# Optimization experiments

Measured on AMD Instinct MI355X. Metric: run time of the kernel, lower is better.

The kernel has to match this reference:

```python
import jax, jax.numpy as jnp
import numpy as np

N = 524288      # number of outer 'batch' steps (acts as the time axis)
S = 1           # inner seq_len
SPIN = 1000
TRAIN = 400000
ML = 2.9086     # hard-coded PET normalizer mean
SL = 1.898      # hard-coded PET normalizer std
SCALE_MR = 500.0


def setup_inputs() -> dict:
    key = jax.random.key(0)
    ks = jax.random.split(key, 16)
    u = lambda k, shape: jax.random.uniform(k, shape, dtype=jnp.float32)
    return {
        "x": u(ks[0], (N, S, 2)),
        "y_obs": u(ks[1], (N, 1)),
        "p_mean": u(ks[2], (1,)),
        "p_std": u(ks[3], (1,)) + 0.5,  # keep away from zero (divisor)
        "weight_r_yom": u(ks[4], (1, 1)),
        "weight_r_ylm": u(ks[5], (1, 1)),
        "weight_r_yfm": u(ks[6], (1, 1)),
        "weight_r_yvm": u(ks[7], (1, 1)),
        "bias_b0_yom": u(ks[8], (1,)),
        "weight_b1_yom": u(ks[9], (1, 1)),
        "bias_b0_ylm": u(ks[10], (1,)),
        "weight_b2_ylm": u(ks[11], (1, 1)),
        "bias_b0_yrm": u(ks[12], (1,)),
        "epoch": 1,       # unused by the forward math
        "time_lag": 0,
    }


def _forward(x, y_obs, p_mean, p_std,
             weight_r_yom, weight_r_ylm, weight_r_yfm, weight_r_yvm,
             bias_b0_yom, weight_b1_yom, bias_b0_ylm, weight_b2_ylm,
             bias_b0_yrm, time_lag):
    n, s, _ = x.shape
    mo = p_mean[0]
    so = p_std[0]
    # hidden_size == 1: all [1,1] matmuls are scalar multiplies
    wb1 = weight_b1_yom[0, 0]
    wb2 = weight_b2_ylm[0, 0]
    b0_yom = bias_b0_yom[0]
    b0_ylm = bias_b0_ylm[0]
    thr = jnp.exp(bias_b0_yrm[0])
    eo = jnp.exp(weight_r_yom[0, 0])
    el = jnp.exp(weight_r_ylm[0, 0])
    ef = jnp.exp(weight_r_yfm[0, 0])
    den = eo + el + ef
    oo1 = eo / den
    ol1 = el / den
    svm = jax.nn.sigmoid(weight_r_yvm[0, 0])

    def cell(c0, u):
        u1, u2 = u[0], u[1]
        oo = oo1 * jax.nn.sigmoid(b0_yom + (c0 - mo) / so * wb1)
        ol = ol1 * jax.nn.sigmoid(b0_ylm + (u2 - ML) / SL * wb2)
        pos = c0 > 0
        safe_c0 = jnp.where(pos, c0, 1.0)
        olc = jnp.where(pos, ol - jax.nn.relu(ol - u2 / safe_c0), ol)
        f = 1.0 - oo - olc
        ov1 = svm * jnp.sign(c0 / SCALE_MR - thr)
        ov = ov1 - jax.nn.relu(ov1 - f)
        c1 = f * c0 + u1 - ov * jnp.abs(c0 - thr * SCALE_MR)
        # recorded quantities use the PRE-update state c0 (as in the torch code)
        outs = jnp.stack([oo * c0, c0, ol * c0, olc * c0, oo, ol, olc, f, ov])
        return c1, outs

    def body(c0, inp_b):
        xb, active = inp_b          # xb: [S,2]
        c1, outs_seq = jax.lax.scan(cell, c0, xb)
        outs = jnp.where(active, outs_seq[-1], 0.0)
        c_next = jnp.where(active, c1, c0)
        return c_next, outs

    active = jnp.arange(n) >= time_lag
    _, O = jax.lax.scan(body, jnp.float32(0.0), (x, active))  # O: [N,9]

    h_n = O[:, 0:1]
    c_n = O[:, 1:2]
    l_n = O[:, 2:3]
    lc_n = O[:, 3:4]
    Gate_oo = O[:, 4:5]
    Gate_ol = O[:, 5:6]
    Gate_olc = O[:, 6:7]
    Gate_f = O[:, 7:8]
    Gate_ov = O[:, 8:9]
    zeros = jnp.zeros_like(h_n)   # bp_n and Gate_ib (ib == 0)
    obsstd = jnp.std(y_obs[SPIN:TRAIN], ddof=1)  # torch.std is unbiased
    obs_std = jnp.where(active[:, None], obsstd, 0.0).astype(x.dtype)
    h_nout = jnp.concatenate([h_n, obs_std], axis=1)
    return (h_n, c_n, l_n, lc_n, zeros, zeros, Gate_oo, Gate_ol, Gate_olc,
            Gate_f, h_nout, obs_std, Gate_ov)


def reference(x, y_obs, p_mean, p_std,
              weight_r_yom, weight_r_ylm, weight_r_yfm, weight_r_yvm,
              bias_b0_yom, weight_b1_yom, bias_b0_ylm, weight_b2_ylm,
              bias_b0_yrm, epoch, time_lag):
    del epoch  # unused by the module's math
    return _forward(x, y_obs, p_mean, p_std,
                    weight_r_yom, weight_r_ylm, weight_r_yfm, weight_r_yvm,
                    bias_b0_yom, weight_b1_yom, bias_b0_ylm, weight_b2_ylm,
                    bias_b0_yrm, time_lag)
```

## Files before the change

### kernel.cpp

```cpp
#include <hip/hip_runtime.h>
#include <math.h>

#define SPIN_  1000
#define TRAIN_ 400000
#define ML_    2.9086f
#define SL_    1.898f
#define SCALE_MR_ 500.0f

#define CHUNK 8
#define BURN  96
#define BLOCK_T 64
#define TILE  (BLOCK_T * CHUNK)
#define WLEN  (TILE + BURN)
#define WPAD  (WLEN + WLEN / 16 + 1)
#define RED_BLOCKS 128
#define AGG_BLOCK  RED_BLOCKS

#define MAGIC_TICKET 0xF00DF00DF00DF00DULL
#define MAGIC_HI     0x5AF00D5AU

__device__ __forceinline__ float rcp_(float x) { return __builtin_amdgcn_rcpf(x); }
__device__ __forceinline__ float sigf_(float x) { return rcp_(1.0f + __expf(-x)); }

struct Params {
    float oo1, ol1, svm, thr, T, k1, a1, k2, a2;
};

__device__ __forceinline__ void step_(float c, float u1, float u2, const Params& P,
                                      float& oo, float& ol, float& olc, float& f,
                                      float& ov, float& c1) {
    oo = P.oo1 * sigf_(fmaf(c, P.k1, P.a1));
    ol = P.ol1 * sigf_(fmaf(u2, P.k2, P.a2));
    float q = u2 * rcp_(c);
    olc = (c > 0.0f) ? fminf(ol, q) : ol;
    f = 1.0f - oo - olc;
    float s = fmaf(c, 1.0f / SCALE_MR_, -P.thr);
    float sg = (s > 0.0f) ? 1.0f : ((s < 0.0f) ? -1.0f : 0.0f);
    ov = fminf(P.svm * sg, f);
    c1 = f * c + u1 - ov * (SCALE_MR_ * fabsf(s));
}

#define ROWP (CHUNK + 1)
#define SSTR (BLOCK_T * ROWP)

__global__ __launch_bounds__(BLOCK_T)
void mcpbrnn_fused_kernel(const float2* __restrict__ x,
                          const float* __restrict__ y,
                          float* __restrict__ out,
                          unsigned long long* __restrict__ W,
                          const float* __restrict__ p_mean,
                          const float* __restrict__ p_std,
                          const float* __restrict__ w_r_yom,
                          const float* __restrict__ w_r_ylm,
                          const float* __restrict__ w_r_yfm,
                          const float* __restrict__ w_r_yvm,
                          const float* __restrict__ b0_yom_p,
                          const float* __restrict__ w_b1_yom,
                          const float* __restrict__ b0_ylm_p,
                          const float* __restrict__ w_b2_ylm,
                          const float* __restrict__ b0_yrm_p,
                          const int* __restrict__ time_lag_p,
                          int n) {
    __shared__ float xu1[WPAD];
    __shared__ float xu2[WPAD];
    __shared__ float lds[9 * SSTR];

    const int tid = threadIdx.x;
    const int bid = blockIdx.x;
    const int base = bid * TILE;
    const int n0 = base + tid * CHUNK;
    const int tl = time_lag_p[0];
    const int N = n;

    if (bid < RED_BLOCKS) {
        const float4* y4 = (const float4*)(y + SPIN_);
        const int n4 = (TRAIN_ - SPIN_) / 4;
        const int per = (n4 + RED_BLOCKS - 1) / RED_BLOCKS;
        int s0 = bid * per;
        int e0 = s0 + per; if (e0 > n4) e0 = n4;
        double s = 0.0, q = 0.0;
        for (int i = s0 + tid; i < e0; i += BLOCK_T) {
            float4 v = y4[i];
            double a = (double)v.x, b = (double)v.y, c = (double)v.z, d = (double)v.w;
            s += a + b + c + d;
            q += a * a + b * b + c * c + d * d;
        }
#pragma unroll
        for (int o = 32; o > 0; o >>= 1) {
            s += __shfl_down(s, o, 64);
            q += __shfl_down(q, o, 64);
        }
        if (tid == 0) {
            atomicExch(&W[2 * bid],     (unsigned long long)__double_as_longlong(s));
            atomicExch(&W[2 * bid + 1], (unsigned long long)__double_as_longlong(q));
            __threadfence();
            atomicExch(&W[256 + bid], MAGIC_TICKET);
        }
    }

    {
        const int f4base = (base - BURN) >> 1;
        for (int k = tid; k < WLEN / 2; k += BLOCK_T) {
            int gk = f4base + k;
            float4 v;
            if (gk >= 0 && 2 * gk + 1 < N) {
                v = ((const float4*)x)[gk];
            } else {
                int i0 = 2 * gk;     if (i0 < 0) i0 = 0; if (i0 > N - 1) i0 = N - 1;
                int i1 = 2 * gk + 1; if (i1 < 0) i1 = 0; if (i1 > N - 1) i1 = N - 1;
                float2 a = x[i0];
                float2 b = x[i1];
                v = make_float4(a.x, a.y, b.x, b.y);
            }
            int p = 2 * k;
            int pp = p + (p >> 4);
            xu1[pp] = v.x; xu2[pp] = v.y;
            int p1 = p + 1;
            int pp1 = p1 + (p1 >> 4);
            xu1[pp1] = v.z; xu2[pp1] = v.w;
        }
    }

    Params P;
    {
        float mo = p_mean[0];
        float so = p_std[0];
        float wb1 = w_b1_yom[0];
        float wb2 = w_b2_ylm[0];
        float b0_yom = b0_yom_p[0];
        float b0_ylm = b0_ylm_p[0];
        P.thr = __expf(b0_yrm_p[0]);
        float eo = __expf(w_r_yom[0]);
        float el = __expf(w_r_ylm[0]);
        float ef = __expf(w_r_yfm[0]);
        float den = eo + el + ef;
        P.oo1 = eo / den;
        P.ol1 = el / den;
        P.svm = sigf_(w_r_yvm[0]);
        P.T = P.thr * SCALE_MR_;
        P.k1 = wb1 / so;
        P.a1 = b0_yom - mo * P.k1;
        P.k2 = wb2 / SL_;
        P.a2 = b0_ylm - ML_ * P.k2;
    }

    __syncthreads();

    const bool full_tile = (base + TILE <= N);
    const bool thread_active = (n0 < N);
    const int pbase = tid * CHUNK;
    const int row = tid * ROWP;

    const int gb0 = n0 - BURN;
    int jthr = tl - gb0; if (jthr < 0) jthr = 0;

    if (thread_active) {
        float c = 0.0f;
#pragma unroll 8
        for (int j = 0; j < BURN; ++j) {
            int p = pbase + j;
            int pp = p + (p >> 4);
            float u1 = xu1[pp];
            float u2 = xu2[pp];
            float oo, ol, olc, f, ov, c1;
            step_(c, u1, u2, P, oo, ol, olc, f, ov, c1);
            c = (j >= jthr) ? c1 : c;
        }

#pragma unroll
        for (int j = 0; j < CHUNK; ++j) {
            int gi = n0 + j;
            if (gi < N) {
                int p = pbase + BURN + j;
                int pp = p + (p >> 4);
                float u1 = xu1[pp];
                float u2 = xu2[pp];
                float oo, ol, olc, f, ov, c1;
                step_(c, u1, u2, P, oo, ol, olc, f, ov, c1);
                bool act = (BURN + j) >= jthr;
                float h = oo * c;
                if (full_tile) {
                    int idx = row + j;
                    lds[0 * SSTR + idx] = act ? h        : 0.0f;
                    lds[1 * SSTR + idx] = act ? c        : 0.0f;
                    lds[2 * SSTR + idx] = act ? ol * c   : 0.0f;
                    lds[3 * SSTR + idx] = act ? olc * c  : 0.0f;
                    lds[4 * SSTR + idx] = act ? oo       : 0.0f;
                    lds[5 * SSTR + idx] = act ? ol       : 0.0f;
                    lds[6 * SSTR + idx] = act ? olc      : 0.0f;
                    lds[7 * SSTR + idx] = act ? f        : 0.0f;
                    lds[8 * SSTR + idx] = act ? ov       : 0.0f;
                } else {
                    float hv = act ? h : 0.0f;
                    out[gi]            = hv;
                    out[N + gi]        = act ? c : 0.0f;
                    out[2 * N + gi]    = act ? ol * c : 0.0f;
                    out[3 * N + gi]    = act ? olc * c : 0.0f;
                    out[4 * N + gi]    = 0.0f;
                    out[5 * N + gi]    = 0.0f;
                    out[6 * N + gi]    = act ? oo : 0.0f;
                    out[7 * N + gi]    = act ? ol : 0.0f;
                    out[8 * N + gi]    = act ? olc : 0.0f;
                    out[9 * N + gi]    = act ? f : 0.0f;
                    out[13 * N + gi]   = act ? ov : 0.0f;
                }
                c = act ? c1 : c;
            }
        }
    }

    __syncthreads();

    if (full_tile) {
        const int soff[9] = {0, 1, 2, 3, 6, 7, 8, 9, 13};
#pragma unroll
        for (int sidx = 0; sidx < 9; ++sidx) {
            float* op = out + soff[sidx] * N + base;
            const float* lp = &lds[sidx * SSTR];
#pragma unroll
            for (int k = 0; k < TILE / (BLOCK_T * 4); ++k) {
                int i = 4 * tid + 256 * k;
                int li = i + (i >> 3);
                float4 v = make_float4(lp[li], lp[li + 1], lp[li + 2], lp[li + 3]);
                *(float4*)(op + i) = v;
            }
        }
        float4 z4 = make_float4(0.f, 0.f, 0.f, 0.f);
#pragma unroll
        for (int k = 0; k < TILE / (BLOCK_T * 4); ++k) {
            int i = 4 * tid + 256 * k;
            *(float4*)(out + 4 * N + base + i) = z4;
            *(float4*)(out + 5 * N + base + i) = z4;
        }
    }

    if (bid == AGG_BLOCK) {
        int b0 = tid, b1 = tid + 64;
        while (atomicAdd(&W[256 + b0], 0ULL) != MAGIC_TICKET) __builtin_amdgcn_s_sleep(8);
        while (atomicAdd(&W[256 + b1], 0ULL) != MAGIC_TICKET) __builtin_amdgcn_s_sleep(8);
        __threadfence();
        double s = __longlong_as_double((long long)atomicAdd(&W[2 * b0], 0ULL))
                 + __longlong_as_double((long long)atomicAdd(&W[2 * b1], 0ULL));
        double q = __longlong_as_double((long long)atomicAdd(&W[2 * b0 + 1], 0ULL))
                 + __longlong_as_double((long long)atomicAdd(&W[2 * b1 + 1], 0ULL));
#pragma unroll
        for (int o = 32; o > 0; o >>= 1) {
            s += __shfl_down(s, o, 64);
            q += __shfl_down(q, o, 64);
        }
        if (tid == 0) {
            double M = (double)(TRAIN_ - SPIN_);
            double var = (q - s * s / M) / (M - 1.0);
            float ostd = (float)sqrt(var > 0.0 ? var : 0.0);
            unsigned long long packed =
                ((unsigned long long)MAGIC_HI << 32) | (unsigned long long)__float_as_uint(ostd);
            __threadfence();
            atomicExch(&W[384], packed);
        }
    }

    float obsstd;
    {
        unsigned long long v = 0;
        if (tid == 0) {
            v = atomicAdd(&W[384], 0ULL);
            while ((unsigned)(v >> 32) != MAGIC_HI) {
                __builtin_amdgcn_s_sleep(16);
                v = atomicAdd(&W[384], 0ULL);
            }
        }
        unsigned lo = (unsigned)v;
        lo = __shfl(lo, 0, 64);
        obsstd = __uint_as_float(lo);
    }

    if (full_tile) {
#pragma unroll
        for (int k = 0; k < TILE / (BLOCK_T * 4); ++k) {
            int i = 4 * tid + 256 * k;
            int gi = base + i;
            float4 sv;
            sv.x = (gi     >= tl) ? obsstd : 0.0f;
            sv.y = (gi + 1 >= tl) ? obsstd : 0.0f;
            sv.z = (gi + 2 >= tl) ? obsstd : 0.0f;
            sv.w = (gi + 3 >= tl) ? obsstd : 0.0f;
            *(float4*)(out + 12 * N + base + i) = sv;
        }
        const float* lp = &lds[0 * SSTR];
#pragma unroll
        for (int k = 0; k < TILE / (BLOCK_T * 2); ++k) {
            int qf = tid + BLOCK_T * k;
            int i = 2 * qf;
            int li = i + (i >> 3);
            int gi = base + i;
            float4 v;
            v.x = lp[li];
            v.y = (gi     >= tl) ? obsstd : 0.0f;
            v.z = lp[li + 1];
            v.w = (gi + 1 >= tl) ? obsstd : 0.0f;
            *(float4*)(out + 10 * N + 2 * base + 4 * qf) = v;
        }
    } else if (thread_active) {
        for (int j = 0; j < CHUNK; ++j) {
            int gi = n0 + j;
            if (gi < N) {
                bool act = gi >= tl;
                float stdv = act ? obsstd : 0.0f;
                out[10 * N + 2 * gi]     = out[gi];
                out[10 * N + 2 * gi + 1] = stdv;
                out[12 * N + gi]         = stdv;
            }
        }
    }
}

extern "C" void kernel_launch(void* const* d_in, const int* in_sizes, int n_in,
                              void* d_out, int out_size, void* d_ws, size_t ws_size,
                              hipStream_t stream) {
    const float* x        = (const float*)d_in[0];
    const float* y_obs    = (const float*)d_in[1];
    const float* p_mean   = (const float*)d_in[2];
    const float* p_std    = (const float*)d_in[3];
    const float* w_r_yom  = (const float*)d_in[4];
    const float* w_r_ylm  = (const float*)d_in[5];
    const float* w_r_yfm  = (const float*)d_in[6];
    const float* w_r_yvm  = (const float*)d_in[7];
    const float* b0_yom   = (const float*)d_in[8];
    const float* wb1_yom  = (const float*)d_in[9];
    const float* b0_ylm   = (const float*)d_in[10];
    const float* wb2_ylm  = (const float*)d_in[11];
    const float* b0_yrm   = (const float*)d_in[12];
    const int*   time_lag = (const int*)d_in[14];

    int n = in_sizes[0] / 2;
    float* out = (float*)d_out;
    unsigned long long* W = (unsigned long long*)d_ws;

    int blocks = (n + TILE - 1) / TILE;
    mcpbrnn_fused_kernel<<<blocks, BLOCK_T, 0, stream>>>(
        (const float2*)x, y_obs, out, W,
        p_mean, p_std, w_r_yom, w_r_ylm, w_r_yfm, w_r_yvm,
        b0_yom, wb1_yom, b0_ylm, wb2_ylm, b0_yrm, time_lag, n);
}
```

Baseline: 108.6 us.

## Precompute input-only gate in staging, add lag-free fast path, widen std reduction

The sigmoid-based ol gate depends only on the input u2, so it is now computed once per staged element while x is loaded into shared memory, instead of in every burn-in and output step. The x channels are interleaved into one padded shared array. A wave-uniform branch skips the time-lag select logic when no thread is lagged. The std reduction is spread over 256 blocks, the ticket and result slots in the workspace move, and the spin-wait sleeps are shorter. The costs are more code size, extra shared memory, and a dependence on the workspace being large enough for the new offsets.

```diff
diff --git a/kernel.cpp b/kernel.cpp
--- a/kernel.cpp
+++ b/kernel.cpp
@@ -12,25 +12,27 @@
 #define BLOCK_T 64
 #define TILE  (BLOCK_T * CHUNK)
 #define WLEN  (TILE + BURN)
-#define WPAD  (WLEN + WLEN / 16 + 1)
-#define RED_BLOCKS 128
+#define RED_BLOCKS 256
 #define AGG_BLOCK  RED_BLOCKS
 
 #define MAGIC_TICKET 0xF00DF00DF00DF00DULL
 #define MAGIC_HI     0x5AF00D5AU
 
+#define XU12SZ (2 * WLEN + (WLEN >> 3) + 2)
+#define XOLSZ  (WLEN + WLEN / 16 + 1)
+
 __device__ __forceinline__ float rcp_(float x) { return __builtin_amdgcn_rcpf(x); }
 __device__ __forceinline__ float sigf_(float x) { return rcp_(1.0f + __expf(-x)); }
 
 struct Params {
-    float oo1, ol1, svm, thr, T, k1, a1, k2, a2;
+    float oo1, ol1, svm, thr, k1, a1, k2, a2;
 };
 
-__device__ __forceinline__ void step_(float c, float u1, float u2, const Params& P,
-                                      float& oo, float& ol, float& olc, float& f,
+__device__ __forceinline__ void step_(float c, float u1, float u2, float ol,
+                                      const Params& P,
+                                      float& oo, float& olc, float& f,
                                       float& ov, float& c1) {
     oo = P.oo1 * sigf_(fmaf(c, P.k1, P.a1));
-    ol = P.ol1 * sigf_(fmaf(u2, P.k2, P.a2));
     float q = u2 * rcp_(c);
     olc = (c > 0.0f) ? fminf(ol, q) : ol;
     f = 1.0f - oo - olc;
@@ -61,8 +63,8 @@
                           const float* __restrict__ b0_yrm_p,
                           const int* __restrict__ time_lag_p,
                           int n) {
-    __shared__ float xu1[WPAD];
-    __shared__ float xu2[WPAD];
+    __shared__ float xu12[XU12SZ];
+    __shared__ float xol[XOLSZ];
     __shared__ float lds[9 * SSTR];
 
     const int tid = threadIdx.x;
@@ -94,30 +96,7 @@
             atomicExch(&W[2 * bid],     (unsigned long long)__double_as_longlong(s));
             atomicExch(&W[2 * bid + 1], (unsigned long long)__double_as_longlong(q));
             __threadfence();
-            atomicExch(&W[256 + bid], MAGIC_TICKET);
-        }
-    }
-
-    {
-        const int f4base = (base - BURN) >> 1;
-        for (int k = tid; k < WLEN / 2; k += BLOCK_T) {
-            int gk = f4base + k;
-            float4 v;
-            if (gk >= 0 && 2 * gk + 1 < N) {
-                v = ((const float4*)x)[gk];
-            } else {
-                int i0 = 2 * gk;     if (i0 < 0) i0 = 0; if (i0 > N - 1) i0 = N - 1;
-                int i1 = 2 * gk + 1; if (i1 < 0) i1 = 0; if (i1 > N - 1) i1 = N - 1;
-                float2 a = x[i0];
-                float2 b = x[i1];
-                v = make_float4(a.x, a.y, b.x, b.y);
-            }
-            int p = 2 * k;
-            int pp = p + (p >> 4);
-            xu1[pp] = v.x; xu2[pp] = v.y;
-            int p1 = p + 1;
-            int pp1 = p1 + (p1 >> 4);
-            xu1[pp1] = v.z; xu2[pp1] = v.w;
+            atomicExch(&W[512 + bid], MAGIC_TICKET);
         }
     }
 
@@ -137,13 +116,37 @@
         P.oo1 = eo / den;
         P.ol1 = el / den;
         P.svm = sigf_(w_r_yvm[0]);
-        P.T = P.thr * SCALE_MR_;
         P.k1 = wb1 / so;
         P.a1 = b0_yom - mo * P.k1;
         P.k2 = wb2 / SL_;
         P.a2 = b0_ylm - ML_ * P.k2;
     }
 
+    {
+        const int f4base = (base - BURN) >> 1;
+        for (int k = tid; k < WLEN / 2; k += BLOCK_T) {
+            int gk = f4base + k;
+            float4 v;
+            if (gk >= 0 && 2 * gk + 1 < N) {
+                v = ((const float4*)x)[gk];
+            } else {
+                int i0 = 2 * gk;     if (i0 < 0) i0 = 0; if (i0 > N - 1) i0 = N - 1;
+                int i1 = 2 * gk + 1; if (i1 < 0) i1 = 0; if (i1 > N - 1) i1 = N - 1;
+                float2 a = x[i0];
+                float2 b = x[i1];
+                v = make_float4(a.x, a.y, b.x, b.y);
+            }
+            int p0 = 2 * k, p1 = 2 * k + 1;
+            int d0 = 2 * p0 + (p0 >> 3);
+            int d1 = 2 * p1 + (p1 >> 3);
+            xu12[d0] = v.x; xu12[d0 + 1] = v.y;
+            xu12[d1] = v.z; xu12[d1 + 1] = v.w;
+            int q0 = p0 + (p0 >> 4), q1 = p1 + (p1 >> 4);
+            xol[q0] = P.ol1 * sigf_(fmaf(v.y, P.k2, P.a2));
+            xol[q1] = P.ol1 * sigf_(fmaf(v.w, P.k2, P.a2));
+        }
+    }
+
     __syncthreads();
 
     const bool full_tile = (base + TILE <= N);
@@ -151,60 +154,110 @@
     const int pbase = tid * CHUNK;
     const int row = tid * ROWP;
 
-    const int gb0 = n0 - BURN;
-    int jthr = tl - gb0; if (jthr < 0) jthr = 0;
+    int jthr = tl - (n0 - BURN); if (jthr < 0) jthr = 0;
+    const bool lagged = __any(jthr > 0);
 
     if (thread_active) {
         float c = 0.0f;
+        if (!lagged) {
 #pragma unroll 8
-        for (int j = 0; j < BURN; ++j) {
-            int p = pbase + j;
-            int pp = p + (p >> 4);
-            float u1 = xu1[pp];
-            float u2 = xu2[pp];
-            float oo, ol, olc, f, ov, c1;
-            step_(c, u1, u2, P, oo, ol, olc, f, ov, c1);
-            c = (j >= jthr) ? c1 : c;
-        }
-
-#pragma unroll
-        for (int j = 0; j < CHUNK; ++j) {
-            int gi = n0 + j;
-            if (gi < N) {
-                int p = pbase + BURN + j;
-                int pp = p + (p >> 4);
-                float u1 = xu1[pp];
-                float u2 = xu2[pp];
-                float oo, ol, olc, f, ov, c1;
-                step_(c, u1, u2, P, oo, ol, olc, f, ov, c1);
-                bool act = (BURN + j) >= jthr;
-                float h = oo * c;
-                if (full_tile) {
-                    int idx = row + j;
-                    lds[0 * SSTR + idx] = act ? h        : 0.0f;
-                    lds[1 * SSTR + idx] = act ? c        : 0.0f;
-                    lds[2 * SSTR + idx] = act ? ol * c   : 0.0f;
-                    lds[3 * SSTR + idx] = act ? olc * c  : 0.0f;
-                    lds[4 * SSTR + idx] = act ? oo       : 0.0f;
-                    lds[5 * SSTR + idx] = act ? ol       : 0.0f;
-                    lds[6 * SSTR + idx] = act ? olc      : 0.0f;
-                    lds[7 * SSTR + idx] = act ? f        : 0.0f;
-                    lds[8 * SSTR + idx] = act ? ov       : 0.0f;
-                } else {
-                    float hv = act ? h : 0.0f;
-                    out[gi]            = hv;
-                    out[N + gi]        = act ? c : 0.0f;
-                    out[2 * N + gi]    = act ? ol * c : 0.0f;
-                    out[3 * N + gi]    = act ? olc * c : 0.0f;
-                    out[4 * N + gi]    = 0.0f;
-                    out[5 * N + gi]    = 0.0f;
-                    out[6 * N + gi]    = act ? oo : 0.0f;
-                    out[7 * N + gi]    = act ? ol : 0.0f;
-                    out[8 * N + gi]    = act ? olc : 0.0f;
-                    out[9 * N + gi]    = act ? f : 0.0f;
-                    out[13 * N + gi]   = act ? ov : 0.0f;
+            for (int j = 0; j < BURN; ++j) {
+                int p = pbase + j;
+                int d = 2 * p + (p >> 3);
+                int qq = p + (p >> 4);
+                float u1 = xu12[d], u2 = xu12[d + 1], ol = xol[qq];
+                float oo, olc, f, ov, c1;
+                step_(c, u1, u2, ol, P, oo, olc, f, ov, c1);
+                c = c1;
+            }
+#pragma unroll
+            for (int j = 0; j < CHUNK; ++j) {
+                int gi = n0 + j;
+                if (gi < N) {
+                    int p = pbase + BURN + j;
+                    int d = 2 * p + (p >> 3);
+                    int qq = p + (p >> 4);
+                    float u1 = xu12[d], u2 = xu12[d + 1], ol = xol[qq];
+                    float oo, olc, f, ov, c1;
+                    step_(c, u1, u2, ol, P, oo, olc, f, ov, c1);
+                    float h = oo * c;
+                    if (full_tile) {
+                        int idx = row + j;
+                        lds[0 * SSTR + idx] = h;
+                        lds[1 * SSTR + idx] = c;
+                        lds[2 * SSTR + idx] = ol * c;
+                        lds[3 * SSTR + idx] = olc * c;
+                        lds[4 * SSTR + idx] = oo;
+                        lds[5 * SSTR + idx] = ol;
+                        lds[6 * SSTR + idx] = olc;
+                        lds[7 * SSTR + idx] = f;
+                        lds[8 * SSTR + idx] = ov;
+                    } else {
+                        out[gi]            = h;
+                        out[N + gi]        = c;
+                        out[2 * N + gi]    = ol * c;
+                        out[3 * N + gi]    = olc * c;
+                        out[4 * N + gi]    = 0.0f;
+                        out[5 * N + gi]    = 0.0f;
+                        out[6 * N + gi]    = oo;
+                        out[7 * N + gi]    = ol;
+                        out[8 * N + gi]    = olc;
+                        out[9 * N + gi]    = f;
+                        out[13 * N + gi]   = ov;
+                    }
+                    c = c1;
                 }
-                c = act ? c1 : c;
+            }
+        } else {
+#pragma unroll 8
+            for (int j = 0; j < BURN; ++j) {
+                int p = pbase + j;
+                int d = 2 * p + (p >> 3);
+                int qq = p + (p >> 4);
+                float u1 = xu12[d], u2 = xu12[d + 1], ol = xol[qq];
+                float oo, olc, f, ov, c1;
+                step_(c, u1, u2, ol, P, oo, olc, f, ov, c1);
+                c = (j >= jthr) ? c1 : c;
+            }
+#pragma unroll
+            for (int j = 0; j < CHUNK; ++j) {
+                int gi = n0 + j;
+                if (gi < N) {
+                    int p = pbase + BURN + j;
+                    int d = 2 * p + (p >> 3);
+                    int qq = p + (p >> 4);
+                    float u1 = xu12[d], u2 = xu12[d + 1], ol = xol[qq];
+                    float oo, olc, f, ov, c1;
+                    step_(c, u1, u2, ol, P, oo, olc, f, ov, c1);
+                    bool act = (BURN + j) >= jthr;
+                    float h = oo * c;
+                    if (full_tile) {
+                        int idx = row + j;
+                        lds[0 * SSTR + idx] = act ? h        : 0.0f;
+                        lds[1 * SSTR + idx] = act ? c        : 0.0f;
+                        lds[2 * SSTR + idx] = act ? ol * c   : 0.0f;
+                        lds[3 * SSTR + idx] = act ? olc * c  : 0.0f;
+                        lds[4 * SSTR + idx] = act ? oo       : 0.0f;
+                        lds[5 * SSTR + idx] = act ? ol       : 0.0f;
+                        lds[6 * SSTR + idx] = act ? olc      : 0.0f;
+                        lds[7 * SSTR + idx] = act ? f        : 0.0f;
+                        lds[8 * SSTR + idx] = act ? ov       : 0.0f;
+                    } else {
+                        float hv = act ? h : 0.0f;
+                        out[gi]            = hv;
+                        out[N + gi]        = act ? c : 0.0f;
+                        out[2 * N + gi]    = act ? ol * c : 0.0f;
+                        out[3 * N + gi]    = act ? olc * c : 0.0f;
+                        out[4 * N + gi]    = 0.0f;
+                        out[5 * N + gi]    = 0.0f;
+                        out[6 * N + gi]    = act ? oo : 0.0f;
+                        out[7 * N + gi]    = act ? ol : 0.0f;
+                        out[8 * N + gi]    = act ? olc : 0.0f;
+                        out[9 * N + gi]    = act ? f : 0.0f;
+                        out[13 * N + gi]   = act ? ov : 0.0f;
+                    }
+                    c = act ? c1 : c;
+                }
             }
         }
     }
@@ -235,14 +288,17 @@
     }
 
     if (bid == AGG_BLOCK) {
-        int b0 = tid, b1 = tid + 64;
-        while (atomicAdd(&W[256 + b0], 0ULL) != MAGIC_TICKET) __builtin_amdgcn_s_sleep(8);
-        while (atomicAdd(&W[256 + b1], 0ULL) != MAGIC_TICKET) __builtin_amdgcn_s_sleep(8);
+#pragma unroll
+        for (int r = tid; r < RED_BLOCKS; r += BLOCK_T) {
+            while (atomicAdd(&W[512 + r], 0ULL) != MAGIC_TICKET) __builtin_amdgcn_s_sleep(2);
+        }
         __threadfence();
-        double s = __longlong_as_double((long long)atomicAdd(&W[2 * b0], 0ULL))
-                 + __longlong_as_double((long long)atomicAdd(&W[2 * b1], 0ULL));
-        double q = __longlong_as_double((long long)atomicAdd(&W[2 * b0 + 1], 0ULL))
-                 + __longlong_as_double((long long)atomicAdd(&W[2 * b1 + 1], 0ULL));
+        double s = 0.0, q = 0.0;
+#pragma unroll
+        for (int r = tid; r < RED_BLOCKS; r += BLOCK_T) {
+            s += __longlong_as_double((long long)atomicAdd(&W[2 * r], 0ULL));
+            q += __longlong_as_double((long long)atomicAdd(&W[2 * r + 1], 0ULL));
+        }
 #pragma unroll
         for (int o = 32; o > 0; o >>= 1) {
             s += __shfl_down(s, o, 64);
@@ -255,7 +311,7 @@
             unsigned long long packed =
                 ((unsigned long long)MAGIC_HI << 32) | (unsigned long long)__float_as_uint(ostd);
             __threadfence();
-            atomicExch(&W[384], packed);
+            atomicExch(&W[768], packed);
         }
     }
 
@@ -263,10 +319,10 @@
     {
         unsigned long long v = 0;
         if (tid == 0) {
-            v = atomicAdd(&W[384], 0ULL);
+            v = atomicAdd(&W[768], 0ULL);
             while ((unsigned)(v >> 32) != MAGIC_HI) {
-                __builtin_amdgcn_s_sleep(16);
-                v = atomicAdd(&W[384], 0ULL);
+                __builtin_amdgcn_s_sleep(2);
+                v = atomicAdd(&W[768], 0ULL);
             }
         }
         unsigned lo = (unsigned)v;
```

Result: slower. 112.9 us (+4.0%).
